# Optimization experiments

Measured on AMD Instinct MI355X. Metric: run time of the kernel, lower is better.

The kernel has to match this reference:

```python
import jax, jax.numpy as jnp
import numpy as np
from jax import lax

DN = ('NCHW', 'OIHW', 'NCHW')


def conv2d(x, w, b, stride, pad):
    y = lax.conv_general_dilated(x, w, (stride, stride), [(pad, pad), (pad, pad)],
                                 dimension_numbers=DN)
    return y + b[None, :, None, None]


def conv2d_transpose(x, w, b):
    # k=4, s=2, p=1 transposed conv: lhs_dilation=2, padding k-1-p=2.
    # w is stored directly as OIHW for this dilated conv (reference params).
    y = lax.conv_general_dilated(x, w, (1, 1), [(2, 2), (2, 2)],
                                 lhs_dilation=(2, 2), dimension_numbers=DN)
    return y + b[None, :, None, None]


def setup_inputs() -> dict:
    key = jax.random.key(0)
    ks = jax.random.split(key, 16)
    D, K = 64, 512  # embedding_dim, num_embeddings
    C1, C2 = 128, 256

    def w(k, shape, fan_in):
        return (jax.random.normal(k, shape, jnp.float32) / np.sqrt(fan_in)).astype(jnp.float32)

    inp = {
        'x':   jax.random.normal(ks[0], (8, 3, 256, 256), jnp.float32),
        # encoder: two stride-2 conv stages (k=4,s=2,p=1) + ReLU
        'ew1': w(ks[1], (C1, 3, 4, 4), 3 * 16),   'eb1': jnp.zeros((C1,), jnp.float32),
        'ew2': w(ks[2], (C2, C1, 4, 4), C1 * 16), 'eb2': jnp.zeros((C2,), jnp.float32),
        # pre_vq 1x1 conv: C2 -> D
        'pvw': w(ks[3], (D, C2, 1, 1), C2),       'pvb': jnp.zeros((D,), jnp.float32),
        # codebook, uniform(-1/K, 1/K) as in the torch init
        'emb': jax.random.uniform(ks[4], (K, D), jnp.float32, -1.0 / K, 1.0 / K),
        # post_vq 3x3 conv: D -> C2
        'qvw': w(ks[5], (C2, D, 3, 3), D * 9),    'qvb': jnp.zeros((C2,), jnp.float32),
        # decoder: two stride-2 transposed conv stages
        'dw1': w(ks[6], (C1, C2, 4, 4), C2 * 16), 'db1': jnp.zeros((C1,), jnp.float32),
        'dw2': w(ks[7], (3, C1, 4, 4), C1 * 16),  'db2': jnp.zeros((3,), jnp.float32),
    }
    return inp


def vector_quantize(z_e, emb, commitment_cost):
    # z_e: [B, D, H, W] -> [B, H, W, D]
    inputs = jnp.transpose(z_e, (0, 2, 3, 1))
    B, H, W, D = inputs.shape
    K = emb.shape[0]
    flat = inputs.reshape(-1, D)                                   # [N, D]
    dist = (jnp.sum(flat * flat, axis=1, keepdims=True)
            + jnp.sum(emb * emb, axis=1)
            - 2.0 * jnp.matmul(flat, emb.T))                        # [N, K]
    idx = jnp.argmin(dist, axis=1)                                  # [N]
    encodings = jax.nn.one_hot(idx, K, dtype=flat.dtype)            # [N, K]
    quantized = emb[idx].reshape(B, H, W, D)                        # gather == encodings @ emb

    e_latent_loss = jnp.mean((lax.stop_gradient(quantized) - inputs) ** 2)
    q_latent_loss = jnp.mean((quantized - lax.stop_gradient(inputs)) ** 2)
    loss = q_latent_loss + commitment_cost * e_latent_loss

    quantized_st = inputs + lax.stop_gradient(quantized - inputs)   # straight-through
    avg_probs = jnp.mean(encodings, axis=0)
    perplexity = jnp.exp(-jnp.sum(avg_probs * jnp.log(avg_probs + 1e-10)))
    return loss, jnp.transpose(quantized_st, (0, 3, 1, 2)), perplexity, encodings


def reference(x, ew1, eb1, ew2, eb2, pvw, pvb, emb, qvw, qvb, dw1, db1, dw2, db2):
    commitment_cost = 0.25
    # encode
    h = jax.nn.relu(conv2d(x, ew1, eb1, 2, 1))    # [8,128,128,128]
    h = jax.nn.relu(conv2d(h, ew2, eb2, 2, 1))    # [8,256,64,64]
    z_e = conv2d(h, pvw, pvb, 1, 0)               # [8,64,64,64]
    # vector quantize
    loss, quantized, perplexity, _ = vector_quantize(z_e, emb, commitment_cost)
    # decode
    g = conv2d(quantized, qvw, qvb, 1, 1)         # [8,256,64,64]
    g = jax.nn.relu(conv2d_transpose(g, dw1, db1))  # [8,128,128,128]
    x_recon = conv2d_transpose(g, dw2, db2)       # [8,3,256,256]
    return (loss, x_recon, perplexity)
```

## Files before the change

kernel.cpp:

```cpp
#include <hip/hip_runtime.h>
#include <math.h>

typedef unsigned short u16;
typedef unsigned int uint;
typedef __attribute__((ext_vector_type(8))) short bh8;
typedef __attribute__((ext_vector_type(4))) float f32x4;

#define DEV __device__ __forceinline__

DEV u16 f2bf(float x) {
  uint u = __builtin_bit_cast(uint, x);
  return (u16)((u + 0x7FFFu + ((u >> 16) & 1u)) >> 16);
}
DEV float bf2f(u16 h) { return __builtin_bit_cast(float, (uint)h << 16); }

DEV int xcd_swz(int bid, int nb) {
  int c = nb >> 3;
  return (bid & 7) * c + (bid >> 3);
}

__global__ __launch_bounds__(256, 4) void conv1_f32(const float* __restrict__ src,
                                                    const float* __restrict__ Bt,
                                                    const float* __restrict__ bias,
                                                    uint* __restrict__ outu) {
  __shared__ __align__(16) float As[16*64];
  __shared__ __align__(16) float Bs[16*64];

  const int t = threadIdx.x;
  const int bid = (int)blockIdx.x;
  const int nt = bid & 1, m = bid >> 1;
  const int pl = t & 63, kb = t >> 6;
  const int p = m*64 + pl;
  const int n = p >> 14, h = (p >> 7) & 127, w = p & 127;
  const int ti = t & 15, tj = t >> 4;

  float acc[4][4];
  #pragma unroll
  for (int i = 0; i < 4; ++i)
    #pragma unroll
    for (int j = 0; j < 4; ++j) acc[i][j] = 0.f;

  for (int k0 = 0; k0 < 48; k0 += 16) {
    #pragma unroll
    for (int jj = 0; jj < 4; ++jj) {
      int kr = jj*4 + kb, k = k0 + kr;
      int ic = k >> 4, r = k & 15;
      int ih = 2*h - 1 + (r >> 2), iw = 2*w - 1 + (r & 3);
      As[kr*64 + pl] = ((unsigned)ih < 256u && (unsigned)iw < 256u)
        ? src[((n*3 + ic) << 16) + (ih << 8) + iw] : 0.f;
    }
    {
      int kr = t >> 4, c4 = t & 15;
      ((float4*)Bs)[kr*16 + c4] =
          *((const float4*)(Bt + (size_t)(k0 + kr)*128 + nt*64) + c4);
    }
    __syncthreads();
    #pragma unroll
    for (int kk = 0; kk < 16; ++kk) {
      float a[4], b[4];
      *(float4*)&a[0] = *(const float4*)&As[kk*64 + ti*4];
      *(float4*)&b[0] = *(const float4*)&Bs[kk*64 + tj*4];
      #pragma unroll
      for (int i = 0; i < 4; ++i)
        #pragma unroll
        for (int j = 0; j < 4; ++j)
          acc[i][j] += a[i]*b[j];
    }
    __syncthreads();
  }

  const int nn = m >> 8, hh = (m >> 1) & 127;
  const int woff2 = (m & 1) * 32;
  #pragma unroll
  for (int j = 0; j < 4; ++j) {
    const int oc = nt*64 + tj*4 + j;
    uint pk[4];
    #pragma unroll
    for (int q = 0; q < 4; ++q) {
      float v = fmaxf(acc[q][j] + bias[oc], 0.f);
      u16 hi = f2bf(v);
      u16 lo = f2bf(v - bf2f(hi));
      pk[q] = (uint)hi | ((uint)lo << 16);
    }
    uint* bp = outu + (size_t)(nn*128 + oc)*16384 + hh*128;
    *(uint2*)(bp + woff2 + ti*2)      = make_uint2(pk[0], pk[2]);
    *(uint2*)(bp + 64 + woff2 + ti*2) = make_uint2(pk[1], pk[3]);
  }
}

__global__ __launch_bounds__(256, 2) void conv2_mfma3(const uint* __restrict__ h1u,
                                                      const u16* __restrict__ Bh,
                                                      const u16* __restrict__ Bl,
                                                      const float* __restrict__ bias,
                                                      float* __restrict__ out) {
  __shared__ __align__(16) u16 Ah[128*72 + 32];
  __shared__ __align__(16) u16 Al[128*72 + 32];
  __shared__ __align__(16) u16 Bhs[128*72 + 32];
  __shared__ __align__(16) u16 Bls[128*72 + 32];

  const int t = threadIdx.x;
  const int bid = xcd_swz((int)blockIdx.x, (int)gridDim.x);
  const int nt = bid & 1, mt = bid >> 1;
  const int pl = t & 127, kb = t >> 7;
  const int p = mt*128 + pl;
  const int n = p >> 12, h = (p >> 6) & 63, w = p & 63;
  const int lane = t & 63, wv = t >> 6;
  const int lr = lane & 15, lg = lane >> 4;
  const int wm = wv & 1, wn = wv >> 1;

  int off[4]; uint mskd[4];
  off[0] = 64 + w - 1; mskd[0] = (w >= 1)  ? ~0u : 0u;
  off[1] = w;          mskd[1] = ~0u;
  off[2] = 64 + w;     mskd[2] = ~0u;
  off[3] = w + 1;      mskd[3] = (w <= 62) ? ~0u : 0u;

  f32x4 acc[4][4];
  #pragma unroll
  for (int fm = 0; fm < 4; ++fm)
    #pragma unroll
    for (int fn = 0; fn < 4; ++fn)
      #pragma unroll
      for (int q = 0; q < 4; ++q) acc[fm][fn][q] = 0.f;

  const int aw = pl*72 + kb*32;

  for (int k0 = 0; k0 < 2048; k0 += 64) {
    const int dy = k0 >> 9, icb = (k0 >> 2) & 127;
    const int ih = 2*h - 1 + dy;
    const uint mih = ((unsigned)ih < 128u) ? ~0u : 0u;
    const uint* pb = h1u + (size_t)(n*128 + icb + kb*8)*16384
                        + (((unsigned)ih < 128u) ? ih : 0)*128;
    uint m2[4];
    #pragma unroll
    for (int dx = 0; dx < 4; ++dx) m2[dx] = mskd[dx] & mih;

    uint raw[32];
    #pragma unroll
    for (int c = 0; c < 8; ++c)
      #pragma unroll
      for (int dx = 0; dx < 4; ++dx)
        raw[c*4 + dx] = pb[c*16384 + off[dx]] & m2[dx];

    uint hi16[16], lo16[16];
    #pragma unroll
    for (int q = 0; q < 16; ++q) {
      uint a = raw[2*q], b = raw[2*q+1];
      hi16[q] = (a & 0xffffu) | (b << 16);
      lo16[q] = (a >> 16) | (b & 0xffff0000u);
    }
    __syncthreads();
    #pragma unroll
    for (int i = 0; i < 4; ++i) {
      *(uint4*)&Ah[aw + i*8] = *(uint4*)&hi16[4*i];
      *(uint4*)&Al[aw + i*8] = *(uint4*)&lo16[4*i];
    }
    #pragma unroll
    for (int i = 0; i < 4; ++i) {
      int id = i*256 + t, oc = id >> 3, ch = id & 7;
      size_t bo = (size_t)(nt*128 + oc)*2048 + k0 + ch*8;
      *(uint4*)&Bhs[oc*72 + ch*8] = *(const uint4*)(Bh + bo);
      *(uint4*)&Bls[oc*72 + ch*8] = *(const uint4*)(Bl + bo);
    }
    __syncthreads();

    #pragma unroll
    for (int ks = 0; ks < 2; ++ks) {
      bh8 afh[4], afl[4];
      #pragma unroll
      for (int fm = 0; fm < 4; ++fm) {
        const int r = (wm*64 + fm*16 + lr)*72 + ks*32 + lg*8;
        afh[fm] = *(const bh8*)&Ah[r];
        afl[fm] = *(const bh8*)&Al[r];
      }
      #pragma unroll
      for (int fn = 0; fn < 4; ++fn) {
        const int r = (wn*64 + fn*16 + lr)*72 + ks*32 + lg*8;
        bh8 bfh = *(const bh8*)&Bhs[r];
        bh8 bfl = *(const bh8*)&Bls[r];
        #pragma unroll
        for (int fm = 0; fm < 4; ++fm) {
          acc[fm][fn] = __builtin_amdgcn_mfma_f32_16x16x32_bf16(afh[fm], bfh, acc[fm][fn], 0,0,0);
          acc[fm][fn] = __builtin_amdgcn_mfma_f32_16x16x32_bf16(afl[fm], bfh, acc[fm][fn], 0,0,0);
          acc[fm][fn] = __builtin_amdgcn_mfma_f32_16x16x32_bf16(afh[fm], bfl, acc[fm][fn], 0,0,0);
        }
      }
    }
  }

  #pragma unroll
  for (int fm = 0; fm < 4; ++fm) {
    const int pq = mt*128 + wm*64 + fm*16 + lg*4;
    const int nn = pq >> 12, hwq = pq & 4095;
    #pragma unroll
    for (int fn = 0; fn < 4; ++fn) {
      const int oc = nt*128 + wn*64 + fn*16 + lr;
      const float bv = bias[oc];
      float v0 = fmaxf(acc[fm][fn][0] + bv, 0.f);
      float v1 = fmaxf(acc[fm][fn][1] + bv, 0.f);
      float v2 = fmaxf(acc[fm][fn][2] + bv, 0.f);
      float v3 = fmaxf(acc[fm][fn][3] + bv, 0.f);
      *(float4*)(out + (((size_t)(nn*256 + oc)) << 12) + hwq) = make_float4(v0,v1,v2,v3);
    }
  }
}

__global__ __launch_bounds__(256, 2) void prevq_vq(const float* __restrict__ h2,
                                                   const float* __restrict__ btp,
                                                   const float* __restrict__ pvb,
                                                   const float* __restrict__ emb,
                                                   const u16* __restrict__ Ebh,
                                                   const u16* __restrict__ Ebl,
                                                   const float* __restrict__ enrm,
                                                   uint* __restrict__ qz32,
                                                   int* __restrict__ hist,
                                                   float* __restrict__ loss_sum) {
  __shared__ __align__(16) char SMEM[75776];
  float* Zs    = (float*)SMEM;
  u16*   Zh    = (u16*)(SMEM + 17408);
  u16*   Zl    = (u16*)(SMEM + 26624);
  u16*   Eh    = (u16*)(SMEM + 35840);
  u16*   El    = (u16*)(SMEM + 54272);
  float* nrmS  = (float*)(SMEM + 72704);
  float* wredv = (float*)(SMEM + 73216);
  int*   wredi = (int*)(SMEM + 74240);
  int*   sIdx  = (int*)(SMEM + 75264);
  float* As    = (float*)(SMEM + 35840);
  float* Bs    = (float*)(SMEM + 35840 + 4096);

  const int t = threadIdx.x;
  const int base = (int)blockIdx.x * 64;
  const int n = base >> 12, hwb = base & 4095;
  const int ti = t & 15, tj = t >> 4;

  {
    const int pl = t & 63, kb = t >> 6;
    const int hw = hwb + pl;
    float acc[4][4];
    #pragma unroll
    for (int i = 0; i < 4; ++i)
      #pragma unroll
      for (int j = 0; j < 4; ++j) acc[i][j] = 0.f;

    for (int k0 = 0; k0 < 256; k0 += 16) {
      #pragma unroll
      for (int jj = 0; jj < 4; ++jj) {
        int kr = jj*4 + kb;
        As[kr*64 + pl] = h2[((size_t)(n*256 + k0 + kr) << 12) + hw];
      }
      {
        int kr = t >> 4, c4 = t & 15;
        ((float4*)Bs)[kr*16 + c4] = *((const float4*)(btp + (size_t)(k0 + kr)*64) + c4);
      }
      __syncthreads();
      #pragma unroll
      for (int kk = 0; kk < 16; ++kk) {
        float a[4], b[4];
        *(float4*)&a[0] = *(const float4*)&As[kk*64 + ti*4];
        *(float4*)&b[0] = *(const float4*)&Bs[kk*64 + tj*4];
        #pragma unroll
        for (int i = 0; i < 4; ++i)
          #pragma unroll
          for (int j = 0; j < 4; ++j)
            acc[i][j] += a[i]*b[j];
      }
      __syncthreads();
    }
    #pragma unroll
    for (int j = 0; j < 4; ++j) {
      const int d = tj*4 + j;
      const float bvv = pvb[d];
      #pragma unroll
      for (int i = 0; i < 4; ++i) {
        const int px = ti*4 + i;
        float z = acc[i][j] + bvv;
        Zs[d*68 + px] = z;
        u16 h = f2bf(z);
        Zh[px*72 + d] = h;
        Zl[px*72 + d] = f2bf(z - bf2f(h));
      }
    }
  }

  const int lane = t & 63, wv = t >> 6;
  const int lr = lane & 15, lg = lane >> 4;

  float bv2[4][4]; int bi2[4][4];
  #pragma unroll
  for (int fm = 0; fm < 4; ++fm)
    #pragma unroll
    for (int q = 0; q < 4; ++q) { bv2[fm][q] = 3.402823466e38f; bi2[fm][q] = 0; }

  for (int c = 0; c < 4; ++c) {
    __syncthreads();
    #pragma unroll
    for (int i = 0; i < 4; ++i) {
      int id = i*256 + t, row = id >> 3, ch = id & 7;
      *(uint4*)&Eh[row*72 + ch*8] = *(const uint4*)(Ebh + (size_t)(c*128 + row)*64 + ch*8);
      *(uint4*)&El[row*72 + ch*8] = *(const uint4*)(Ebl + (size_t)(c*128 + row)*64 + ch*8);
    }
    if (t < 128) nrmS[t] = enrm[c*128 + t];
    __syncthreads();

    f32x4 acc2[4][2];
    #pragma unroll
    for (int fm = 0; fm < 4; ++fm)
      #pragma unroll
      for (int fn = 0; fn < 2; ++fn)
        #pragma unroll
        for (int q = 0; q < 4; ++q) acc2[fm][fn][q] = 0.f;

    #pragma unroll
    for (int ks = 0; ks < 2; ++ks) {
      bh8 ah[4], al[4];
      #pragma unroll
      for (int fm = 0; fm < 4; ++fm) {
        const int r = (fm*16 + lr)*72 + ks*32 + lg*8;
        ah[fm] = *(const bh8*)&Zh[r];
        al[fm] = *(const bh8*)&Zl[r];
      }
      #pragma unroll
      for (int fn = 0; fn < 2; ++fn) {
        const int r = (wv*32 + fn*16 + lr)*72 + ks*32 + lg*8;
        bh8 bh_ = *(const bh8*)&Eh[r];
        bh8 bl_ = *(const bh8*)&El[r];
        #pragma unroll
        for (int fm = 0; fm < 4; ++fm) {
          acc2[fm][fn] = __builtin_amdgcn_mfma_f32_16x16x32_bf16(ah[fm], bh_, acc2[fm][fn], 0,0,0);
          acc2[fm][fn] = __builtin_amdgcn_mfma_f32_16x16x32_bf16(al[fm], bh_, acc2[fm][fn], 0,0,0);
          acc2[fm][fn] = __builtin_amdgcn_mfma_f32_16x16x32_bf16(ah[fm], bl_, acc2[fm][fn], 0,0,0);
        }
      }
    }
    #pragma unroll
    for (int fn = 0; fn < 2; ++fn) {
      const int code = c*128 + wv*32 + fn*16 + lr;
      const float nv = nrmS[wv*32 + fn*16 + lr];
      #pragma unroll
      for (int fm = 0; fm < 4; ++fm)
        #pragma unroll
        for (int q = 0; q < 4; ++q) {
          float d = nv - 2.f*acc2[fm][fn][q];
          if (d < bv2[fm][q]) { bv2[fm][q] = d; bi2[fm][q] = code; }
        }
    }
  }

  #pragma unroll
  for (int fm = 0; fm < 4; ++fm)
    #pragma unroll
    for (int q = 0; q < 4; ++q) {
      float v = bv2[fm][q]; int ix = bi2[fm][q];
      #pragma unroll
      for (int m = 1; m < 16; m <<= 1) {
        float ov = __shfl_xor(v, m, 64);
        int   oi = __shfl_xor(ix, m, 64);
        if (ov < v || (ov == v && oi < ix)) { v = ov; ix = oi; }
      }
      if (lr == 0) {
        const int px = fm*16 + lg*4 + q;
        wredv[wv*64 + px] = v;
        wredi[wv*64 + px] = ix;
      }
    }
  __syncthreads();
  if (t < 64) {
    float best = 3.402823466e38f; int bid = 0x7fffffff;
    #pragma unroll
    for (int w2 = 0; w2 < 4; ++w2) {
      float v = wredv[w2*64 + t]; int ix = wredi[w2*64 + t];
      if (v < best || (v == best && ix < bid)) { best = v; bid = ix; }
    }
    sIdx[t] = bid;
  }
  __syncthreads();

  const int px = t & 63, grp = t >> 6;
  const int ix = sIdx[px];
  const float* er = emb + (size_t)ix * 64 + grp*16;
  uint* qb = qz32 + ((size_t)(n*32 + grp*8))*4096 + hwb + px;
  float ls = 0.f;
  #pragma unroll
  for (int dp = 0; dp < 8; ++dp) {
    float e0 = er[2*dp], e1 = er[2*dp + 1];
    float z0 = Zs[(grp*16 + 2*dp)*68 + px];
    float z1 = Zs[(grp*16 + 2*dp + 1)*68 + px];
    float d0 = e0 - z0, d1 = e1 - z1;
    ls += d0*d0 + d1*d1;
    qb[(size_t)dp * 4096] = (uint)f2bf(e0) | ((uint)f2bf(e1) << 16);
  }
  if (t < 64) atomicAdd(&hist[ix], 1);
  #pragma unroll
  for (int o = 32; o; o >>= 1) ls += __shfl_down(ls, o, 64);
  if ((t & 63) == 0) atomicAdd(loss_sum, ls);
}

__global__ void finalize_kernel(const int* __restrict__ hist,
                                const float* __restrict__ loss_sum,
                                float* __restrict__ out_loss,
                                float* __restrict__ out_perp) {
  __shared__ float red[512];
  int t = threadIdx.x;
  float pr = (float)hist[t] * (1.f/32768.f);
  red[t] = pr * logf(pr + 1e-10f);
  __syncthreads();
  for (int s = 256; s; s >>= 1) {
    if (t < s) red[t] += red[t + s];
    __syncthreads();
  }
  if (t == 0) {
    out_loss[0] = 1.25f * loss_sum[0] * (1.f/2097152.f);
    out_perp[0] = expf(-red[0]);
  }
}

enum { M_POSTVQ, M_DECONV1, M_DECONV2 };

template<int MODE>
__global__ __launch_bounds__(256, 4) void dec_mfma128(const uint* __restrict__ srcu,
                                                      const u16* __restrict__ Bt,
                                                      const float* __restrict__ bias,
                                                      uint* __restrict__ out32) {
  constexpr int K = (MODE == M_POSTVQ) ? 576 : 1024;
  __shared__ __align__(16) u16 As[128*72 + 32];
  __shared__ __align__(16) u16 Bs[128*72 + 32];

  const int t = threadIdx.x;
  int bid = xcd_swz((int)blockIdx.x, (int)gridDim.x);
  int par = 0, nt = 0, mt;
  if constexpr (MODE == M_DECONV1) { par = bid & 3; mt = bid >> 2; }
  else                             { nt = bid & 1;  mt = bid >> 1; }
  const u16* Brow = Bt + (size_t)((MODE == M_DECONV1) ? par*128 : nt*128) * K;

  const int pl = t & 127, kb = t >> 7;
  const int p = mt*128 + pl;
  const int n = p >> 12, h = (p >> 6) & 63, w = p & 63;
  const int lane = t & 63, wv = t >> 6;
  const int lr = lane & 15, lg = lane >> 4;
  const int wm = wv & 1, wn = wv >> 1;

  f32x4 acc[4][4];
  #pragma unroll
  for (int fm = 0; fm < 4; ++fm)
    #pragma unroll
    for (int fn = 0; fn < 4; ++fn)
      #pragma unroll
      for (int q = 0; q < 4; ++q) acc[fm][fn][q] = 0.f;

  const int aw = pl*72 + kb*32;

  for (int k0 = 0; k0 < K; k0 += 64) {
    const uint* up; bool ok;
    if constexpr (MODE == M_POSTVQ) {
      int r = k0 >> 6, kh = r / 3, kw = r - 3*kh;
      int ih = h - 1 + kh, iw = w - 1 + kw;
      ok = ((unsigned)ih < 64u) && ((unsigned)iw < 64u);
      up = srcu + ((size_t)(n*32 + kb*16)) * 4096
                + (ok ? ((ih << 6) + iw) : 0);
    } else {
      int j = k0 >> 8, icb = k0 & 255;
      int j1 = j >> 1, j0 = j & 1;
      int py = par >> 1, px = par & 1;
      int ih = h + py - 1 + j1, iw = w + px - 1 + j0;
      ok = ((unsigned)ih < 64u) && ((unsigned)iw < 64u);
      up = srcu + ((size_t)(n*128 + (icb >> 1) + kb*16)) * 4096
                + (ok ? ((ih << 6) + iw) : 0);
    }
    uint raw[16];
    #pragma unroll
    for (int i = 0; i < 16; ++i)
      raw[i] = ok ? up[(size_t)i * 4096] : 0u;

    __syncthreads();
    #pragma unroll
    for (int i = 0; i < 4; ++i)
      *(uint4*)&As[aw + i*8] =
          make_uint4(raw[4*i], raw[4*i+1], raw[4*i+2], raw[4*i+3]);

    #pragma unroll
    for (int i = 0; i < 4; ++i) {
      int id = i*256 + t, oc = id >> 3, ch = id & 7;
      *(uint4*)&Bs[oc*72 + ch*8] = *(const uint4*)(Brow + (size_t)oc*K + k0 + ch*8);
    }
    __syncthreads();

    #pragma unroll
    for (int ks = 0; ks < 2; ++ks) {
      bh8 af[4];
      #pragma unroll
      for (int fm = 0; fm < 4; ++fm)
        af[fm] = *(const bh8*)&As[(wm*64 + fm*16 + lr)*72 + ks*32 + lg*8];
      #pragma unroll
      for (int fn = 0; fn < 4; ++fn) {
        bh8 bf = *(const bh8*)&Bs[(wn*64 + fn*16 + lr)*72 + ks*32 + lg*8];
        #pragma unroll
        for (int fm = 0; fm < 4; ++fm)
          acc[fm][fn] = __builtin_amdgcn_mfma_f32_16x16x32_bf16(af[fm], bf, acc[fm][fn], 0, 0, 0);
      }
    }
  }

  const bool evn = !(lr & 1);
  #pragma unroll
  for (int fm = 0; fm < 4; ++fm) {
    const int pq = mt*128 + wm*64 + fm*16 + lg*4;
    const int nn = pq >> 12, hwq = pq & 4095;
    #pragma unroll
    for (int fn = 0; fn < 4; ++fn) {
      const int oc = nt*128 + wn*64 + fn*16 + lr;
      const float bvv = bias[oc];
      float v[4];
      #pragma unroll
      for (int q = 0; q < 4; ++q) {
        v[q] = acc[fm][fn][q] + bvv;
        if constexpr (MODE == M_DECONV1) v[q] = fmaxf(v[q], 0.f);
      }
      float pv[4];
      #pragma unroll
      for (int q = 0; q < 4; ++q) pv[q] = __shfl_xor(v[q], 1, 64);
      uint pk[4];
      #pragma unroll
      for (int q = 0; q < 4; ++q) {
        u16 a = f2bf(evn ? v[q] : pv[q]);
        u16 b = f2bf(evn ? pv[q] : v[q]);
        pk[q] = (uint)a | ((uint)b << 16);
      }
      size_t pbase;
      if constexpr (MODE == M_POSTVQ)
        pbase = ((size_t)(nn*128 + (oc >> 1))) * 4096 + hwq;
      else
        pbase = ((size_t)((nn*4 + par)*64 + (oc >> 1))) * 4096 + hwq;
      if (evn) *(uint2*)(out32 + pbase)     = make_uint2(pk[0], pk[1]);
      else     *(uint2*)(out32 + pbase + 2) = make_uint2(pk[2], pk[3]);
    }
  }
}

__global__ __launch_bounds__(256, 4) void deconv2_mfma(const uint* __restrict__ srcu,
                                                       const u16* __restrict__ Bt,
                                                       const float* __restrict__ bias,
                                                       float* __restrict__ outf) {
  constexpr int K = 512, BN = 16;
  __shared__ __align__(16) u16 As[128 * 72];
  __shared__ __align__(16) u16 Bs[BN * 72];

  const int t = threadIdx.x;
  int bid = xcd_swz((int)blockIdx.x, (int)gridDim.x);
  int par = bid & 3; bid >>= 2;
  const int mt = bid;
  const u16* Brow = Bt + (size_t)par * BN * K;

  const int pl = t & 127, kb = t >> 7;
  const int p = mt * 128 + pl;
  const int n = p >> 14, h = (p >> 7) & 127, w = p & 127;

  const int lane = t & 63, wv = t >> 6;
  const int lr = lane & 15, lg = lane >> 4;

  f32x4 acc[2];
  #pragma unroll
  for (int fm = 0; fm < 2; ++fm)
    #pragma unroll
    for (int q = 0; q < 4; ++q) acc[fm][q] = 0.f;

  for (int k0 = 0; k0 < K; k0 += 64) {
    int tap = k0 >> 7, icb = k0 & 127;
    int j1 = tap >> 1, j0 = tap & 1;
    int qy = par >> 1, qx = par & 1;
    int ih = h - 1 + qy + j1, iw = w - 1 + qx + j0;
    bool ok = ((unsigned)ih < 128u) && ((unsigned)iw < 128u);
    int ipar = ((ih & 1) << 1) | (iw & 1);
    const uint* up = srcu + ((size_t)((n*4 + ipar)*64 + (icb >> 1) + kb*16)) * 4096
                          + (ok ? (((ih >> 1) << 6) + (iw >> 1)) : 0);
    uint raw[16];
    #pragma unroll
    for (int i = 0; i < 16; ++i)
      raw[i] = ok ? up[(size_t)i * 4096] : 0u;

    __syncthreads();
    #pragma unroll
    for (int i = 0; i < 4; ++i)
      *(uint4*)&As[pl*72 + kb*32 + i*8] =
          make_uint4(raw[4*i], raw[4*i+1], raw[4*i+2], raw[4*i+3]);
    {
      int id = t;
      if (id < BN*8) {
        int oc = id >> 3, ch = id & 7;
        *(uint4*)&Bs[oc*72 + ch*8] = *(const uint4*)(Brow + (size_t)oc*K + k0 + ch*8);
      }
    }
    __syncthreads();

    #pragma unroll
    for (int ks = 0; ks < 2; ++ks) {
      bh8 af[2];
      #pragma unroll
      for (int fm = 0; fm < 2; ++fm)
        af[fm] = *(const bh8*)&As[(wv*32 + fm*16 + lr)*72 + ks*32 + lg*8];
      bh8 bf = *(const bh8*)&Bs[lr*72 + ks*32 + lg*8];
      #pragma unroll
      for (int fm = 0; fm < 2; ++fm)
        acc[fm] = __builtin_amdgcn_mfma_f32_16x16x32_bf16(af[fm], bf, acc[fm], 0, 0, 0);
    }
  }

  #pragma unroll
  for (int fm = 0; fm < 2; ++fm) {
    const int pq = mt*128 + wv*32 + fm*16 + lg*4;
    const int oc = lr;
    if (oc < 3) {
      const float bvv = bias[oc];
      const int nn = pq >> 14;
      const int hq = (pq >> 7) & 127, wq = pq & 127;
      const int qy = par >> 1, qx = par & 1;
      const int oh = 2*hq + qy;
      float* ob = outf + (((size_t)(nn*3 + oc)) << 16) + (oh << 8) + qx;
      ob[2*wq]     = acc[fm][0] + bvv;
      ob[2*wq + 2] = acc[fm][1] + bvv;
      ob[2*wq + 4] = acc[fm][2] + bvv;
      ob[2*wq + 6] = acc[fm][3] + bvv;
    }
  }
}

__global__ void prep_enc(const float* __restrict__ ew1, const float* __restrict__ ew2,
                         const float* __restrict__ pvw, const float* __restrict__ emb,
                         float* bt1, u16* bt2h, u16* bt2l, float* btp,
                         u16* Ebh, u16* Ebl, float* enrm) {
  int i = blockIdx.x * 256 + threadIdx.x;
  if (i < 6144) {
    int k = i >> 7, oc = i & 127;
    bt1[i] = ew1[oc*48 + k];
  } else if ((i -= 6144) < 524288) {
    int oc = i >> 11, k = i & 2047;
    int dy = k >> 9, ic = (k >> 2) & 127, dx = k & 3;
    float v = ew2[oc*2048 + ic*16 + dy*4 + dx];
    u16 hi = f2bf(v);
    bt2h[i] = hi;
    bt2l[i] = f2bf(v - bf2f(hi));
  } else if ((i -= 524288) < 16384) {
    int k = i >> 6, oc = i & 63;
    btp[i] = pvw[oc*256 + k];
  } else if ((i -= 16384) < 32768) {
    float v = emb[i];
    u16 hi = f2bf(v);
    Ebh[i] = hi;
    Ebl[i] = f2bf(v - bf2f(hi));
  } else if ((i -= 32768) < 512) {
    float s = 0.f;
    const float* er = emb + (size_t)i * 64;
    #pragma unroll
    for (int d = 0; d < 64; ++d) s += er[d]*er[d];
    enrm[i] = s;
  }
}

__global__ void prep_dec(const float* __restrict__ qvw, const float* __restrict__ dw1,
                         const float* __restrict__ dw2,
                         u16* btq, u16* btd, u16* btd2) {
  int i = blockIdx.x * 256 + threadIdx.x;
  if (i < 147456) {
    int oc = i / 576, rem = i - oc*576, r = rem >> 6, ic = rem & 63;
    btq[i] = f2bf(qvw[oc*576 + ic*9 + r]);
  } else if ((i -= 147456) < 524288) {
    int pr = i >> 17, oc = (i >> 10) & 127, j = (i >> 8) & 3, ic = i & 255;
    int py = pr >> 1, px = pr & 1, j1 = j >> 1, j0 = j & 1;
    btd[i] = f2bf(dw1[oc*4096 + ic*16 + (py + 2*j1)*4 + (px + 2*j0)]);
  } else if ((i -= 524288) < 32768) {
    int q = i >> 13, oc = (i >> 9) & 15, tap = (i >> 7) & 3, ic = i & 127;
    int qy = q >> 1, qx = q & 1, j1 = tap >> 1, j0 = tap & 1;
    btd2[i] = (oc < 3) ? f2bf(dw2[oc*2048 + ic*16 + (qy + 2*j1)*4 + (qx + 2*j0)]) : (u16)0;
  }
}

extern "C" void kernel_launch(void* const* d_in, const int* in_sizes, int n_in,
                              void* d_out, int out_size, void* d_ws, size_t ws_size,
                              hipStream_t stream) {
  (void)in_sizes; (void)n_in; (void)ws_size;
  const float* x   = (const float*)d_in[0];
  const float* ew1 = (const float*)d_in[1];
  const float* eb1 = (const float*)d_in[2];
  const float* ew2 = (const float*)d_in[3];
  const float* eb2 = (const float*)d_in[4];
  const float* pvw = (const float*)d_in[5];
  const float* pvb = (const float*)d_in[6];
  const float* emb = (const float*)d_in[7];
  const float* qvw = (const float*)d_in[8];
  const float* qvb = (const float*)d_in[9];
  const float* dw1 = (const float*)d_in[10];
  const float* db1 = (const float*)d_in[11];
  const float* dw2 = (const float*)d_in[12];
  const float* db2 = (const float*)d_in[13];
  float* out = (float*)d_out;

  char* ws = (char*)d_ws;
  uint*  h1u  = (uint*) (ws);
  float* h2   = (float*)(ws + 67108864);
  uint*  qz32 = (uint*) (ws + 109051904);
  int*   hist = (int*)  (ws + 113246208);
  float* lsum = (float*)(ws + 113248256);
  float* bt1  = (float*)(ws + 113248320);
  float* btp  = (float*)(ws + 113272896);
  u16*   bt2h = (u16*)  (ws + 113338432);
  u16*   bt2l = (u16*)  (ws + 114387008);
  u16*   btq  = (u16*)  (ws + 115435584);
  u16*   btd  = (u16*)  (ws + 115730496);
  u16*   btd2 = (u16*)  (ws + 116779072);
  u16*   Ebh  = (u16*)  (ws + 116844608);
  u16*   Ebl  = (u16*)  (ws + 116910144);
  float* enrm = (float*)(ws + 116975680);
  uint* g32  = (uint*)(ws + 67108864);
  uint* g232 = (uint*)ws;

  hipMemsetAsync(hist, 0, 2048 + 64, stream);
  prep_enc<<<2266, 256, 0, stream>>>(ew1, ew2, pvw, emb, bt1, bt2h, bt2l, btp, Ebh, Ebl, enrm);
  prep_dec<<<2752, 256, 0, stream>>>(qvw, dw1, dw2, btq, btd, btd2);

  conv1_f32<<<4096, 256, 0, stream>>>(x, bt1, eb1, h1u);
  conv2_mfma3<<<512, 256, 0, stream>>>(h1u, bt2h, bt2l, eb2, h2);

  prevq_vq<<<512, 256, 0, stream>>>(h2, btp, pvb, emb, Ebh, Ebl, enrm, qz32, hist, lsum);
  finalize_kernel<<<1, 512, 0, stream>>>(hist, lsum, out, out + (out_size - 1));

  dec_mfma128<M_POSTVQ> <<<512,  256, 0, stream>>>(qz32, btq, qvb, g32);
  dec_mfma128<M_DECONV1><<<1024, 256, 0, stream>>>(g32, btd, db1, g232);
  deconv2_mfma<<<4096, 256, 0, stream>>>(g232, btd2, db2, out + 1);
}
```

Measured before the change: 390.1 us.

## Move conv1 to split-bf16 MFMA and merge prep kernels with memset

Replaces the scalar fp32 first encoder conv with a 3-term split-bf16 MFMA GEMM (hi*hi + lo*hi + hi*lo) over 128-pixel by 128-channel tiles, with K padded from 48 to 64. Conv1 weights are now pre-split into hi/lo bf16. The two weight-prep kernels and the histogram/loss memset are folded into one prep kernel to cut launch overhead. The split-bf16 product drops the lo*lo term, so results differ slightly from fp32, and K padding adds a quarter more MMA work.

```diff
diff --git a/kernel.cpp b/kernel.cpp
--- a/kernel.cpp
+++ b/kernel.cpp
@@ -19,72 +19,112 @@
   return (bid & 7) * c + (bid >> 3);
 }
 
-__global__ __launch_bounds__(256, 4) void conv1_f32(const float* __restrict__ src,
-                                                    const float* __restrict__ Bt,
-                                                    const float* __restrict__ bias,
-                                                    uint* __restrict__ outu) {
-  __shared__ __align__(16) float As[16*64];
-  __shared__ __align__(16) float Bs[16*64];
+__global__ __launch_bounds__(256, 2) void conv1_mfma3(const float* __restrict__ src,
+                                                      const u16* __restrict__ B1h,
+                                                      const u16* __restrict__ B1l,
+                                                      const float* __restrict__ bias,
+                                                      uint* __restrict__ outu) {
+  __shared__ __align__(16) u16 Ah[128*72 + 32];
+  __shared__ __align__(16) u16 Al[128*72 + 32];
+  __shared__ __align__(16) u16 Bh[128*72 + 32];
+  __shared__ __align__(16) u16 Bl[128*72 + 32];
 
   const int t = threadIdx.x;
-  const int bid = (int)blockIdx.x;
-  const int nt = bid & 1, m = bid >> 1;
-  const int pl = t & 63, kb = t >> 6;
-  const int p = m*64 + pl;
+  const int mt = xcd_swz((int)blockIdx.x, (int)gridDim.x);
+  const int pl = t & 127, kb = t >> 7;
+  const int p = mt*128 + pl;
   const int n = p >> 14, h = (p >> 7) & 127, w = p & 127;
-  const int ti = t & 15, tj = t >> 4;
-
-  float acc[4][4];
-  #pragma unroll
-  for (int i = 0; i < 4; ++i)
-    #pragma unroll
-    for (int j = 0; j < 4; ++j) acc[i][j] = 0.f;
-
-  for (int k0 = 0; k0 < 48; k0 += 16) {
-    #pragma unroll
-    for (int jj = 0; jj < 4; ++jj) {
-      int kr = jj*4 + kb, k = k0 + kr;
-      int ic = k >> 4, r = k & 15;
-      int ih = 2*h - 1 + (r >> 2), iw = 2*w - 1 + (r & 3);
-      As[kr*64 + pl] = ((unsigned)ih < 256u && (unsigned)iw < 256u)
-        ? src[((n*3 + ic) << 16) + (ih << 8) + iw] : 0.f;
-    }
-    {
-      int kr = t >> 4, c4 = t & 15;
-      ((float4*)Bs)[kr*16 + c4] =
-          *((const float4*)(Bt + (size_t)(k0 + kr)*128 + nt*64) + c4);
-    }
-    __syncthreads();
-    #pragma unroll
-    for (int kk = 0; kk < 16; ++kk) {
-      float a[4], b[4];
-      *(float4*)&a[0] = *(const float4*)&As[kk*64 + ti*4];
-      *(float4*)&b[0] = *(const float4*)&Bs[kk*64 + tj*4];
-      #pragma unroll
-      for (int i = 0; i < 4; ++i)
-        #pragma unroll
-        for (int j = 0; j < 4; ++j)
-          acc[i][j] += a[i]*b[j];
-    }
-    __syncthreads();
-  }
-
-  const int nn = m >> 8, hh = (m >> 1) & 127;
-  const int woff2 = (m & 1) * 32;
-  #pragma unroll
-  for (int j = 0; j < 4; ++j) {
-    const int oc = nt*64 + tj*4 + j;
-    uint pk[4];
-    #pragma unroll
-    for (int q = 0; q < 4; ++q) {
-      float v = fmaxf(acc[q][j] + bias[oc], 0.f);
-      u16 hi = f2bf(v);
-      u16 lo = f2bf(v - bf2f(hi));
-      pk[q] = (uint)hi | ((uint)lo << 16);
-    }
-    uint* bp = outu + (size_t)(nn*128 + oc)*16384 + hh*128;
-    *(uint2*)(bp + woff2 + ti*2)      = make_uint2(pk[0], pk[2]);
-    *(uint2*)(bp + 64 + woff2 + ti*2) = make_uint2(pk[1], pk[3]);
+  const int lane = t & 63, wv = t >> 6;
+  const int lr = lane & 15, lg = lane >> 4;
+  const int wm = wv & 1, wn = wv >> 1;
+
+  uint hi16[16], lo16[16];
+  #pragma unroll
+  for (int q = 0; q < 16; ++q) {
+    uint hh = 0, ll = 0;
+    #pragma unroll
+    for (int e = 0; e < 2; ++e) {
+      const int k = kb*32 + q*2 + e;
+      float val = 0.f;
+      if (k < 48) {
+        const int ic = k >> 4, r = k & 15;
+        const int ih = 2*h - 1 + (r >> 2), iw = 2*w - 1 + (r & 3);
+        if ((unsigned)ih < 256u && (unsigned)iw < 256u)
+          val = src[((n*3 + ic) << 16) + (ih << 8) + iw];
+      }
+      u16 hi = f2bf(val);
+      u16 lo = f2bf(val - bf2f(hi));
+      hh |= (uint)hi << (16*e);
+      ll |= (uint)lo << (16*e);
+    }
+    hi16[q] = hh; lo16[q] = ll;
+  }
+  const int aw = pl*72 + kb*32;
+  #pragma unroll
+  for (int i = 0; i < 4; ++i) {
+    *(uint4*)&Ah[aw + i*8] = *(uint4*)&hi16[4*i];
+    *(uint4*)&Al[aw + i*8] = *(uint4*)&lo16[4*i];
+  }
+  #pragma unroll
+  for (int i = 0; i < 4; ++i) {
+    int id = i*256 + t, oc = id >> 3, ch = id & 7;
+    *(uint4*)&Bh[oc*72 + ch*8] = *(const uint4*)(B1h + (size_t)oc*64 + ch*8);
+    *(uint4*)&Bl[oc*72 + ch*8] = *(const uint4*)(B1l + (size_t)oc*64 + ch*8);
+  }
+  __syncthreads();
+
+  f32x4 acc[4][4];
+  #pragma unroll
+  for (int fm = 0; fm < 4; ++fm)
+    #pragma unroll
+    for (int fn = 0; fn < 4; ++fn)
+      #pragma unroll
+      for (int q = 0; q < 4; ++q) acc[fm][fn][q] = 0.f;
+
+  #pragma unroll
+  for (int ks = 0; ks < 2; ++ks) {
+    bh8 afh[4], afl[4];
+    #pragma unroll
+    for (int fm = 0; fm < 4; ++fm) {
+      const int r = (wm*64 + fm*16 + lr)*72 + ks*32 + lg*8;
+      afh[fm] = *(const bh8*)&Ah[r];
+      afl[fm] = *(const bh8*)&Al[r];
+    }
+    #pragma unroll
+    for (int fn = 0; fn < 4; ++fn) {
+      const int r = (wn*64 + fn*16 + lr)*72 + ks*32 + lg*8;
+      bh8 bfh = *(const bh8*)&Bh[r];
+      bh8 bfl = *(const bh8*)&Bl[r];
+      #pragma unroll
+      for (int fm = 0; fm < 4; ++fm) {
+        acc[fm][fn] = __builtin_amdgcn_mfma_f32_16x16x32_bf16(afh[fm], bfh, acc[fm][fn], 0,0,0);
+        acc[fm][fn] = __builtin_amdgcn_mfma_f32_16x16x32_bf16(afl[fm], bfh, acc[fm][fn], 0,0,0);
+        acc[fm][fn] = __builtin_amdgcn_mfma_f32_16x16x32_bf16(afh[fm], bfl, acc[fm][fn], 0,0,0);
+      }
+    }
+  }
+
+  #pragma unroll
+  for (int fm = 0; fm < 4; ++fm) {
+    const int pq = mt*128 + wm*64 + fm*16 + lg*4;
+    const int nn = pq >> 14, hh2 = (pq >> 7) & 127, ww = pq & 127;
+    const int wh = ww >> 1;
+    #pragma unroll
+    for (int fn = 0; fn < 4; ++fn) {
+      const int oc = wn*64 + fn*16 + lr;
+      const float bv = bias[oc];
+      uint pk[4];
+      #pragma unroll
+      for (int q = 0; q < 4; ++q) {
+        float v = fmaxf(acc[fm][fn][q] + bv, 0.f);
+        u16 hi = f2bf(v);
+        u16 lo = f2bf(v - bf2f(hi));
+        pk[q] = (uint)hi | ((uint)lo << 16);
+      }
+      uint* bp = outu + (size_t)(nn*128 + oc)*16384 + hh2*128;
+      *(uint2*)(bp + wh)      = make_uint2(pk[0], pk[2]);
+      *(uint2*)(bp + 64 + wh) = make_uint2(pk[1], pk[3]);
+    }
   }
 }
 
@@ -622,15 +662,22 @@
   }
 }
 
-__global__ void prep_enc(const float* __restrict__ ew1, const float* __restrict__ ew2,
+__global__ void prep_all(const float* __restrict__ ew1, const float* __restrict__ ew2,
                          const float* __restrict__ pvw, const float* __restrict__ emb,
-                         float* bt1, u16* bt2h, u16* bt2l, float* btp,
-                         u16* Ebh, u16* Ebl, float* enrm) {
+                         const float* __restrict__ qvw, const float* __restrict__ dw1,
+                         const float* __restrict__ dw2,
+                         u16* bt1h, u16* bt1l, u16* bt2h, u16* bt2l, float* btp,
+                         u16* Ebh, u16* Ebl, float* enrm,
+                         u16* btq, u16* btd, u16* btd2,
+                         int* hist, float* lsum) {
   int i = blockIdx.x * 256 + threadIdx.x;
-  if (i < 6144) {
-    int k = i >> 7, oc = i & 127;
-    bt1[i] = ew1[oc*48 + k];
-  } else if ((i -= 6144) < 524288) {
+  if (i < 8192) {
+    int oc = i >> 6, k = i & 63;
+    float v = (k < 48) ? ew1[oc*48 + k] : 0.f;
+    u16 hi = f2bf(v);
+    bt1h[i] = hi;
+    bt1l[i] = f2bf(v - bf2f(hi));
+  } else if ((i -= 8192) < 524288) {
     int oc = i >> 11, k = i & 2047;
     int dy = k >> 9, ic = (k >> 2) & 127, dx = k & 3;
     float v = ew2[oc*2048 + ic*16 + dy*4 + dx];
@@ -651,14 +698,7 @@
     #pragma unroll
     for (int d = 0; d < 64; ++d) s += er[d]*er[d];
     enrm[i] = s;
-  }
-}
-
-__global__ void prep_dec(const float* __restrict__ qvw, const float* __restrict__ dw1,
-                         const float* __restrict__ dw2,
-                         u16* btq, u16* btd, u16* btd2) {
-  int i = blockIdx.x * 256 + threadIdx.x;
-  if (i < 147456) {
+  } else if ((i -= 512) < 147456) {
     int oc = i / 576, rem = i - oc*576, r = rem >> 6, ic = rem & 63;
     btq[i] = f2bf(qvw[oc*576 + ic*9 + r]);
   } else if ((i -= 147456) < 524288) {
@@ -669,6 +709,9 @@
     int q = i >> 13, oc = (i >> 9) & 15, tap = (i >> 7) & 3, ic = i & 127;
     int qy = q >> 1, qx = q & 1, j1 = tap >> 1, j0 = tap & 1;
     btd2[i] = (oc < 3) ? f2bf(dw2[oc*2048 + ic*16 + (qy + 2*j1)*4 + (qx + 2*j0)]) : (u16)0;
+  } else if ((i -= 32768) < 528) {
+    if (i < 512) hist[i] = 0;
+    else         lsum[i - 512] = 0.f;
   }
 }
 
@@ -698,24 +741,25 @@
   uint*  qz32 = (uint*) (ws + 109051904);
   int*   hist = (int*)  (ws + 113246208);
   float* lsum = (float*)(ws + 113248256);
-  float* bt1  = (float*)(ws + 113248320);
-  float* btp  = (float*)(ws + 113272896);
-  u16*   bt2h = (u16*)  (ws + 113338432);
-  u16*   bt2l = (u16*)  (ws + 114387008);
-  u16*   btq  = (u16*)  (ws + 115435584);
-  u16*   btd  = (u16*)  (ws + 115730496);
-  u16*   btd2 = (u16*)  (ws + 116779072);
-  u16*   Ebh  = (u16*)  (ws + 116844608);
-  u16*   Ebl  = (u16*)  (ws + 116910144);
-  float* enrm = (float*)(ws + 116975680);
+  u16*   bt1h = (u16*)  (ws + 113248320);
+  u16*   bt1l = (u16*)  (ws + 113264704);
+  float* btp  = (float*)(ws + 113281088);
+  u16*   bt2h = (u16*)  (ws + 113346624);
+  u16*   bt2l = (u16*)  (ws + 114395200);
+  u16*   btq  = (u16*)  (ws + 115443776);
+  u16*   btd  = (u16*)  (ws + 115738688);
+  u16*   btd2 = (u16*)  (ws + 116787264);
+  u16*   Ebh  = (u16*)  (ws + 116852800);
+  u16*   Ebl  = (u16*)  (ws + 116918336);
+  float* enrm = (float*)(ws + 116983872);
   uint* g32  = (uint*)(ws + 67108864);
   uint* g232 = (uint*)ws;
 
-  hipMemsetAsync(hist, 0, 2048 + 64, stream);
-  prep_enc<<<2266, 256, 0, stream>>>(ew1, ew2, pvw, emb, bt1, bt2h, bt2l, btp, Ebh, Ebl, enrm);
-  prep_dec<<<2752, 256, 0, stream>>>(qvw, dw1, dw2, btq, btd, btd2);
-
-  conv1_f32<<<4096, 256, 0, stream>>>(x, bt1, eb1, h1u);
+  prep_all<<<5029, 256, 0, stream>>>(ew1, ew2, pvw, emb, qvw, dw1, dw2,
+                                     bt1h, bt1l, bt2h, bt2l, btp,
+                                     Ebh, Ebl, enrm, btq, btd, btd2, hist, lsum);
+
+  conv1_mfma3<<<1024, 256, 0, stream>>>(x, bt1h, bt1l, eb1, h1u);
   conv2_mfma3<<<512, 256, 0, stream>>>(h1u, bt2h, bt2l, eb2, h2);
 
   prevq_vq<<<512, 256, 0, stream>>>(h2, btp, pvb, emb, Ebh, Ebl, enrm, qz32, hist, lsum);
```

After: 378.1 us. -3.1%, faster.
